# Optimization experiments

Hardware: AMD Instinct MI355X
Metric: run time of the kernel (lower is better)

Reference implementation:

```python
import jax, jax.numpy as jnp
import numpy as np

HEADS = 4
HEAD_DIM = 32
IN_DIM = 128
N_TRIG = 48
N_SPAN = 128


def build_edges(T, S):
    # nodes are (trig r, span c) flattened row-major: n = r*S + c
    N = T * S
    nodes = jnp.arange(N, dtype=jnp.int32)
    r = nodes // S
    c = nodes % S
    # same-row neighbors (includes self loop once): [N, S]
    row_nb = r[:, None] * S + jnp.arange(S, dtype=jnp.int32)[None, :]
    # same-column neighbors excluding own row: [N, T-1]
    t_idx = jnp.arange(T - 1, dtype=jnp.int32)[None, :]
    t = t_idx + (t_idx >= r[:, None]).astype(jnp.int32)
    col_nb = t * S + c[:, None]
    deg = S + T - 1
    src = jnp.concatenate([row_nb, col_nb], axis=1).reshape(-1)  # [N*deg]
    dst = jnp.repeat(nodes, deg)
    return src, dst, N


def gat_conv(x, src, dst, N, W, att_src, att_dst, bias):
    # PyG GATConv (eval mode, dropout off), concat=True.
    # W: [in, H*Hd]; att_src/att_dst: [H, Hd]; bias: [H*Hd]
    h = (x @ W).reshape(N, HEADS, HEAD_DIM)          # [N,H,Hd]
    a_src = jnp.sum(h * att_src[None], axis=-1)      # [N,H]
    a_dst = jnp.sum(h * att_dst[None], axis=-1)      # [N,H]
    e = jax.nn.leaky_relu(a_src[src] + a_dst[dst], negative_slope=0.2)  # [E,H]
    # scatter-softmax over incoming edges per destination node
    m = jax.ops.segment_max(e, dst, num_segments=N)  # [N,H]
    ex = jnp.exp(e - m[dst])
    denom = jax.ops.segment_sum(ex, dst, num_segments=N)
    alpha = ex / denom[dst]                          # [E,H]
    msg = alpha[:, :, None] * h[src]                 # [E,H,Hd]
    out = jax.ops.segment_sum(msg, dst, num_segments=N)  # [N,H,Hd]
    return out.reshape(N, HEADS * HEAD_DIM) + bias[None]


def setup_inputs() -> dict:
    key = jax.random.key(0)
    ks = jax.random.split(key, 9)
    D = IN_DIM
    HD = HEADS * HEAD_DIM
    inp = {
        "pair_embeddings": jax.random.normal(ks[0], (1, N_TRIG, N_SPAN, D), dtype=jnp.float32),
        "W1": jax.random.normal(ks[1], (D, HD), dtype=jnp.float32) * (2.0 / (D + HD)) ** 0.5,
        "att_src1": jax.random.normal(ks[2], (HEADS, HEAD_DIM), dtype=jnp.float32) * 0.1,
        "att_dst1": jax.random.normal(ks[3], (HEADS, HEAD_DIM), dtype=jnp.float32) * 0.1,
        "b1": jnp.zeros((HD,), dtype=jnp.float32),
        "W2": jax.random.normal(ks[4], (HD, HD), dtype=jnp.float32) * (2.0 / (HD + HD)) ** 0.5,
        "att_src2": jax.random.normal(ks[5], (HEADS, HEAD_DIM), dtype=jnp.float32) * 0.1,
        "att_dst2": jax.random.normal(ks[6], (HEADS, HEAD_DIM), dtype=jnp.float32) * 0.1,
        "b2": jnp.zeros((HD,), dtype=jnp.float32),
        "num_trigs_kept": N_TRIG,
        "num_arg_spans_kept": N_SPAN,
    }
    return inp


def reference(pair_embeddings, W1, att_src1, att_dst1, b1, W2, att_src2, att_dst2, b2, num_trigs_kept, num_arg_spans_kept):
    T, S = int(num_trigs_kept), int(num_arg_spans_kept)
    src, dst, N = build_edges(T, S)
    # batch_size == 1: slice and flatten node features
    x = pair_embeddings[0, :T, :S].reshape(N, -1)
    x = jax.nn.elu(gat_conv(x, src, dst, N, W1, att_src1, att_dst1, b1))
    x = jax.nn.elu(gat_conv(x, src, dst, N, W2, att_src2, att_dst2, b2))
    return x
```

## Files before the change

kernel.cpp:

```cpp
#include <hip/hip_runtime.h>

#define T_TRIG 48
#define S_SPAN 128
#define NN (T_TRIG * S_SPAN)
#define D 128

__global__ __launch_bounds__(256) void gemm_att_kernel(
    const float* __restrict__ X, const float* __restrict__ W,
    const float* __restrict__ att_s, const float* __restrict__ att_d,
    float* __restrict__ H, float* __restrict__ asrc, float* __restrict__ adst)
{
    const int tid = threadIdx.x;
    const int tx = tid & 15;
    const int ty = tid >> 4;
    const int i0 = blockIdx.x * 32 + ty * 2;
    const int j0 = tx * 8;

    float acc[2][8];
    #pragma unroll
    for (int a = 0; a < 2; ++a)
        #pragma unroll
        for (int b = 0; b < 8; ++b) acc[a][b] = 0.f;

    const float* x0 = X + (size_t)i0 * D;
    #pragma unroll 4
    for (int k = 0; k < D; k += 4) {
        float4 xa4 = *(const float4*)(x0 + k);
        float4 xb4 = *(const float4*)(x0 + D + k);
        float xa[4] = {xa4.x, xa4.y, xa4.z, xa4.w};
        float xb[4] = {xb4.x, xb4.y, xb4.z, xb4.w};
        #pragma unroll
        for (int kk = 0; kk < 4; ++kk) {
            const float* wr = W + (k + kk) * D + j0;
            float4 w0 = *(const float4*)(wr);
            float4 w1 = *(const float4*)(wr + 4);
            float wv[8] = {w0.x, w0.y, w0.z, w0.w, w1.x, w1.y, w1.z, w1.w};
            #pragma unroll
            for (int jj = 0; jj < 8; ++jj) {
                acc[0][jj] = fmaf(xa[kk], wv[jj], acc[0][jj]);
                acc[1][jj] = fmaf(xb[kk], wv[jj], acc[1][jj]);
            }
        }
    }

    #pragma unroll
    for (int ii = 0; ii < 2; ++ii) {
        float4 o0 = {acc[ii][0], acc[ii][1], acc[ii][2], acc[ii][3]};
        float4 o1 = {acc[ii][4], acc[ii][5], acc[ii][6], acc[ii][7]};
        *(float4*)&H[(size_t)(i0 + ii) * D + j0]     = o0;
        *(float4*)&H[(size_t)(i0 + ii) * D + j0 + 4] = o1;
    }

    const int head = tx >> 2;
    const int dbase = head * 32 + (tx & 3) * 8;
    float asv[8], adv[8];
    #pragma unroll
    for (int jj = 0; jj < 8; ++jj) {
        asv[jj] = att_s[dbase + jj];
        adv[jj] = att_d[dbase + jj];
    }
    #pragma unroll
    for (int ii = 0; ii < 2; ++ii) {
        float ps = 0.f, pd = 0.f;
        #pragma unroll
        for (int jj = 0; jj < 8; ++jj) {
            ps = fmaf(acc[ii][jj], asv[jj], ps);
            pd = fmaf(acc[ii][jj], adv[jj], pd);
        }
        ps += __shfl_xor(ps, 1); ps += __shfl_xor(ps, 2);
        pd += __shfl_xor(pd, 1); pd += __shfl_xor(pd, 2);
        if ((tx & 3) == 0) {
            asrc[(i0 + ii) * 4 + head] = ps;
            adst[(i0 + ii) * 4 + head] = pd;
        }
    }
}

__global__ __launch_bounds__(256) void row_agg_kernel(
    const float* __restrict__ H, const float* __restrict__ asrc,
    const float* __restrict__ adst, float* __restrict__ num_row,
    float* __restrict__ den_row)
{
    __shared__ float sh_h[S_SPAN][32];
    __shared__ float sh_as[S_SPAN];
    const int tid = threadIdx.x;
    const int r = blockIdx.x >> 2;
    const int h = blockIdx.x & 3;
    const int base = r * S_SPAN;

    #pragma unroll
    for (int it = 0; it < 4; ++it) {
        int chunk = tid + it * 256;
        int cp = chunk >> 3, fc = chunk & 7;
        *(float4*)&sh_h[cp][fc * 4] =
            *(const float4*)&H[(size_t)(base + cp) * D + h * 32 + fc * 4];
    }
    if (tid < S_SPAN) sh_as[tid] = asrc[(base + tid) * 4 + h];
    __syncthreads();

    const int fg = tid & 3;
    const int cth = tid >> 2;
    const float ad0 = adst[(base + cth) * 4 + h];
    const float ad1 = adst[(base + cth + 64) * 4 + h];
    float4 n00 = {0,0,0,0}, n01 = {0,0,0,0}, n10 = {0,0,0,0}, n11 = {0,0,0,0};
    float den0 = 0.f, den1 = 0.f;

    #pragma unroll 2
    for (int cp = 0; cp < S_SPAN; ++cp) {
        float a = sh_as[cp];
        float4 h0 = *(float4*)&sh_h[cp][fg * 8];
        float4 h1 = *(float4*)&sh_h[cp][fg * 8 + 4];
        float e0 = a + ad0; e0 = fmaxf(e0, 0.2f * e0);
        float e1 = a + ad1; e1 = fmaxf(e1, 0.2f * e1);
        float w0 = __expf(e0);
        float w1 = __expf(e1);
        den0 += w0; den1 += w1;
        n00.x = fmaf(w0, h0.x, n00.x); n00.y = fmaf(w0, h0.y, n00.y);
        n00.z = fmaf(w0, h0.z, n00.z); n00.w = fmaf(w0, h0.w, n00.w);
        n01.x = fmaf(w0, h1.x, n01.x); n01.y = fmaf(w0, h1.y, n01.y);
        n01.z = fmaf(w0, h1.z, n01.z); n01.w = fmaf(w0, h1.w, n01.w);
        n10.x = fmaf(w1, h0.x, n10.x); n10.y = fmaf(w1, h0.y, n10.y);
        n10.z = fmaf(w1, h0.z, n10.z); n10.w = fmaf(w1, h0.w, n10.w);
        n11.x = fmaf(w1, h1.x, n11.x); n11.y = fmaf(w1, h1.y, n11.y);
        n11.z = fmaf(w1, h1.z, n11.z); n11.w = fmaf(w1, h1.w, n11.w);
    }

    const int n0 = base + cth, n1 = n0 + 64;
    *(float4*)&num_row[(size_t)n0 * D + h * 32 + fg * 8]     = n00;
    *(float4*)&num_row[(size_t)n0 * D + h * 32 + fg * 8 + 4] = n01;
    *(float4*)&num_row[(size_t)n1 * D + h * 32 + fg * 8]     = n10;
    *(float4*)&num_row[(size_t)n1 * D + h * 32 + fg * 8 + 4] = n11;
    if (fg == 0) {
        den_row[n0 * 4 + h] = den0;
        den_row[n1 * 4 + h] = den1;
    }
}

__global__ __launch_bounds__(256) void col_agg_kernel(
    const float* __restrict__ H, const float* __restrict__ asrc,
    const float* __restrict__ adst, const float* __restrict__ num_row,
    const float* __restrict__ den_row, const float* __restrict__ bias,
    float* __restrict__ out)
{
    __shared__ float sh_h[T_TRIG][D];
    __shared__ float sh_as[4][T_TRIG];
    const int c = blockIdx.x;
    const int tid = threadIdx.x;

    #pragma unroll
    for (int it = 0; it < 6; ++it) {
        int chunk = tid + it * 256;
        int t = chunk >> 5, fc = chunk & 31;
        *(float4*)&sh_h[t][fc * 4] =
            *(const float4*)&H[(size_t)(t * S_SPAN + c) * D + fc * 4];
    }
    if (tid < 4 * T_TRIG) {
        int hh = tid / T_TRIG, t = tid - hh * T_TRIG;
        sh_as[hh][t] = asrc[(t * S_SPAN + c) * 4 + hh];
    }
    __syncthreads();

    const int f4g = tid & 31;
    const int tg = tid >> 5;
    const int head = f4g >> 3;

    float4 num[6];
    float den[6], ad[6];
    #pragma unroll
    for (int dd = 0; dd < 6; ++dd) {
        num[dd] = {0,0,0,0};
        den[dd] = 0.f;
        ad[dd] = adst[((tg * 6 + dd) * S_SPAN + c) * 4 + head];
    }

    for (int tp = 0; tp < T_TRIG; ++tp) {
        float a = sh_as[head][tp];
        float4 hv = *(float4*)&sh_h[tp][f4g * 4];
        #pragma unroll
        for (int dd = 0; dd < 6; ++dd) {
            float e = a + ad[dd];
            e = fmaxf(e, 0.2f * e);
            float w = __expf(e);
            w = (tp == tg * 6 + dd) ? 0.f : w;
            den[dd] += w;
            num[dd].x = fmaf(w, hv.x, num[dd].x);
            num[dd].y = fmaf(w, hv.y, num[dd].y);
            num[dd].z = fmaf(w, hv.z, num[dd].z);
            num[dd].w = fmaf(w, hv.w, num[dd].w);
        }
    }

    const float4 b4 = *(const float4*)&bias[f4g * 4];
    #pragma unroll
    for (int dd = 0; dd < 6; ++dd) {
        int n = (tg * 6 + dd) * S_SPAN + c;
        float4 nr = *(const float4*)&num_row[(size_t)n * D + f4g * 4];
        float dr = den_row[n * 4 + head];
        float inv = 1.f / (dr + den[dd]);
        float4 o;
        o.x = (nr.x + num[dd].x) * inv + b4.x;
        o.y = (nr.y + num[dd].y) * inv + b4.y;
        o.z = (nr.z + num[dd].z) * inv + b4.z;
        o.w = (nr.w + num[dd].w) * inv + b4.w;
        o.x = o.x > 0.f ? o.x : (__expf(o.x) - 1.f);
        o.y = o.y > 0.f ? o.y : (__expf(o.y) - 1.f);
        o.z = o.z > 0.f ? o.z : (__expf(o.z) - 1.f);
        o.w = o.w > 0.f ? o.w : (__expf(o.w) - 1.f);
        *(float4*)&out[(size_t)n * D + f4g * 4] = o;
    }
}

extern "C" void kernel_launch(void* const* d_in, const int* in_sizes, int n_in,
                              void* d_out, int out_size, void* d_ws, size_t ws_size,
                              hipStream_t stream)
{
    const float* pe  = (const float*)d_in[0];
    const float* W1  = (const float*)d_in[1];
    const float* as1 = (const float*)d_in[2];
    const float* ad1 = (const float*)d_in[3];
    const float* b1  = (const float*)d_in[4];
    const float* W2  = (const float*)d_in[5];
    const float* as2 = (const float*)d_in[6];
    const float* ad2 = (const float*)d_in[7];
    const float* b2  = (const float*)d_in[8];
    float* out = (float*)d_out;

    float* ws = (float*)d_ws;
    float* H     = ws;
    float* X2    = H + (size_t)NN * D;
    float* numr  = X2 + (size_t)NN * D;
    float* asrcb = numr + (size_t)NN * D;
    float* adstb = asrcb + (size_t)NN * 4;
    float* denb  = adstb + (size_t)NN * 4;

    gemm_att_kernel<<<dim3(NN / 32), dim3(256), 0, stream>>>(pe, W1, as1, ad1, H, asrcb, adstb);
    row_agg_kernel<<<dim3(T_TRIG * 4), dim3(256), 0, stream>>>(H, asrcb, adstb, numr, denb);
    col_agg_kernel<<<dim3(S_SPAN), dim3(256), 0, stream>>>(H, asrcb, adstb, numr, denb, b1, X2);
    gemm_att_kernel<<<dim3(NN / 32), dim3(256), 0, stream>>>(X2, W2, as2, ad2, H, asrcb, adstb);
    row_agg_kernel<<<dim3(T_TRIG * 4), dim3(256), 0, stream>>>(H, asrcb, adstb, numr, denb);
    col_agg_kernel<<<dim3(S_SPAN), dim3(256), 0, stream>>>(H, asrcb, adstb, numr, denb, b2, out);
}
```

Measured before the change: 93.97 us.

## Replace FP32 SIMT GEMM with split-bf16 MFMA GEMM and prepacked weights

Replaces the scalar FMA projection GEMM with a matrix-core kernel that uses bf16 MFMA 16x16x32. Each fp32 operand is split into high and low bf16 parts, and three MFMAs per tile recover near-fp32 accuracy. A small pre-pass kernel packs W1 and W2 into an MFMA-friendly layout in the workspace on every call. The attention dot products are then computed from the MFMA accumulators with cross-lane shuffles. The costs are an extra launch, strided scalar stores of H, and slightly lower precision than true fp32.

```diff
diff --git a/kernel.cpp b/kernel.cpp
--- a/kernel.cpp
+++ b/kernel.cpp
@@ -5,73 +5,123 @@
 #define NN (T_TRIG * S_SPAN)
 #define D 128
 
-__global__ __launch_bounds__(256) void gemm_att_kernel(
-    const float* __restrict__ X, const float* __restrict__ W,
+typedef __attribute__((ext_vector_type(8))) short sh8;
+typedef __attribute__((ext_vector_type(4))) float f32x4;
+
+__device__ inline unsigned short f2bf(float v) {
+    unsigned u = __float_as_uint(v);
+    unsigned r = u + 0x7FFFu + ((u >> 16) & 1u);
+    return (unsigned short)(r >> 16);
+}
+__device__ inline float bf2f(unsigned short b) {
+    return __uint_as_float(((unsigned)b) << 16);
+}
+
+__global__ __launch_bounds__(64) void pack_w_kernel(
+    const float* __restrict__ W1, const float* __restrict__ W2,
+    unsigned short* __restrict__ w1h, unsigned short* __restrict__ w1l,
+    unsigned short* __restrict__ w2h, unsigned short* __restrict__ w2l)
+{
+    const int b = blockIdx.x;
+    const int l = threadIdx.x;
+    const float* W = (b < 8) ? W1 : W2;
+    unsigned short* wh = (b < 8) ? w1h : w2h;
+    unsigned short* wl = (b < 8) ? w1l : w2l;
+    const int nt = b & 7;
+    const int n = nt * 16 + (l & 15);
+    const int kgb = (l >> 4) * 8;
+
+    #pragma unroll
+    for (int kc = 0; kc < 4; ++kc) {
+        unsigned short hb[8], lb[8];
+        #pragma unroll
+        for (int i = 0; i < 8; ++i) {
+            int k = kc * 32 + kgb + i;
+            float v = W[k * D + n];
+            unsigned short h = f2bf(v);
+            hb[i] = h;
+            lb[i] = f2bf(v - bf2f(h));
+        }
+        size_t base = ((size_t)(nt * 4 + kc) * 64 + l) * 8;
+        #pragma unroll
+        for (int i = 0; i < 8; ++i) { wh[base + i] = hb[i]; wl[base + i] = lb[i]; }
+    }
+}
+
+__global__ __launch_bounds__(64) void gemm_mfma_kernel(
+    const float* __restrict__ X,
+    const unsigned short* __restrict__ Wh, const unsigned short* __restrict__ Wl,
     const float* __restrict__ att_s, const float* __restrict__ att_d,
     float* __restrict__ H, float* __restrict__ asrc, float* __restrict__ adst)
 {
-    const int tid = threadIdx.x;
-    const int tx = tid & 15;
-    const int ty = tid >> 4;
-    const int i0 = blockIdx.x * 32 + ty * 2;
-    const int j0 = tx * 8;
-
-    float acc[2][8];
-    #pragma unroll
-    for (int a = 0; a < 2; ++a)
-        #pragma unroll
-        for (int b = 0; b < 8; ++b) acc[a][b] = 0.f;
-
-    const float* x0 = X + (size_t)i0 * D;
-    #pragma unroll 4
-    for (int k = 0; k < D; k += 4) {
-        float4 xa4 = *(const float4*)(x0 + k);
-        float4 xb4 = *(const float4*)(x0 + D + k);
-        float xa[4] = {xa4.x, xa4.y, xa4.z, xa4.w};
-        float xb[4] = {xb4.x, xb4.y, xb4.z, xb4.w};
-        #pragma unroll
-        for (int kk = 0; kk < 4; ++kk) {
-            const float* wr = W + (k + kk) * D + j0;
-            float4 w0 = *(const float4*)(wr);
-            float4 w1 = *(const float4*)(wr + 4);
-            float wv[8] = {w0.x, w0.y, w0.z, w0.w, w1.x, w1.y, w1.z, w1.w};
-            #pragma unroll
-            for (int jj = 0; jj < 8; ++jj) {
-                acc[0][jj] = fmaf(xa[kk], wv[jj], acc[0][jj]);
-                acc[1][jj] = fmaf(xb[kk], wv[jj], acc[1][jj]);
-            }
-        }
-    }
-
-    #pragma unroll
-    for (int ii = 0; ii < 2; ++ii) {
-        float4 o0 = {acc[ii][0], acc[ii][1], acc[ii][2], acc[ii][3]};
-        float4 o1 = {acc[ii][4], acc[ii][5], acc[ii][6], acc[ii][7]};
-        *(float4*)&H[(size_t)(i0 + ii) * D + j0]     = o0;
-        *(float4*)&H[(size_t)(i0 + ii) * D + j0 + 4] = o1;
-    }
-
-    const int head = tx >> 2;
-    const int dbase = head * 32 + (tx & 3) * 8;
-    float asv[8], adv[8];
-    #pragma unroll
-    for (int jj = 0; jj < 8; ++jj) {
-        asv[jj] = att_s[dbase + jj];
-        adv[jj] = att_d[dbase + jj];
-    }
-    #pragma unroll
-    for (int ii = 0; ii < 2; ++ii) {
-        float ps = 0.f, pd = 0.f;
-        #pragma unroll
-        for (int jj = 0; jj < 8; ++jj) {
-            ps = fmaf(acc[ii][jj], asv[jj], ps);
-            pd = fmaf(acc[ii][jj], adv[jj], pd);
-        }
-        ps += __shfl_xor(ps, 1); ps += __shfl_xor(ps, 2);
-        pd += __shfl_xor(pd, 1); pd += __shfl_xor(pd, 2);
-        if ((tx & 3) == 0) {
-            asrc[(i0 + ii) * 4 + head] = ps;
-            adst[(i0 + ii) * 4 + head] = pd;
+    const int l = threadIdx.x;
+    const int mt = blockIdx.x >> 1;
+    const int nh = blockIdx.x & 1;
+    const int c = l & 15;
+    const int kg = l >> 4;
+    const int row0 = mt * 16;
+
+    const sh8* Wh8 = (const sh8*)Wh;
+    const sh8* Wl8 = (const sh8*)Wl;
+
+    f32x4 acc[4] = {f32x4{0,0,0,0}, f32x4{0,0,0,0}, f32x4{0,0,0,0}, f32x4{0,0,0,0}};
+
+    #pragma unroll
+    for (int kc = 0; kc < 4; ++kc) {
+        const float* xp = X + (size_t)(row0 + c) * D + kc * 32 + kg * 8;
+        float4 x0 = *(const float4*)xp;
+        float4 x1 = *(const float4*)(xp + 4);
+        float xs[8] = {x0.x, x0.y, x0.z, x0.w, x1.x, x1.y, x1.z, x1.w};
+        sh8 ah, al;
+        #pragma unroll
+        for (int i = 0; i < 8; ++i) {
+            unsigned short h = f2bf(xs[i]);
+            ah[i] = (short)h;
+            al[i] = (short)f2bf(xs[i] - bf2f(h));
+        }
+        #pragma unroll
+        for (int ntl = 0; ntl < 4; ++ntl) {
+            int ntg = nh * 4 + ntl;
+            sh8 bh = Wh8[(ntg * 4 + kc) * 64 + l];
+            sh8 bl = Wl8[(ntg * 4 + kc) * 64 + l];
+            acc[ntl] = __builtin_amdgcn_mfma_f32_16x16x32_bf16(ah, bh, acc[ntl], 0, 0, 0);
+            acc[ntl] = __builtin_amdgcn_mfma_f32_16x16x32_bf16(al, bh, acc[ntl], 0, 0, 0);
+            acc[ntl] = __builtin_amdgcn_mfma_f32_16x16x32_bf16(ah, bl, acc[ntl], 0, 0, 0);
+        }
+    }
+
+    #pragma unroll
+    for (int ntl = 0; ntl < 4; ++ntl) {
+        #pragma unroll
+        for (int i = 0; i < 4; ++i) {
+            H[(size_t)(row0 + kg * 4 + i) * D + nh * 64 + ntl * 16 + c] = acc[ntl][i];
+        }
+    }
+
+    float asv[4], adv[4];
+    #pragma unroll
+    for (int ntl = 0; ntl < 4; ++ntl) {
+        int d = (nh * 2 + (ntl >> 1)) * 32 + (ntl & 1) * 16 + c;
+        asv[ntl] = att_s[d];
+        adv[ntl] = att_d[d];
+    }
+    #pragma unroll
+    for (int i = 0; i < 4; ++i) {
+        float ps0 = acc[0][i] * asv[0] + acc[1][i] * asv[1];
+        float ps1 = acc[2][i] * asv[2] + acc[3][i] * asv[3];
+        float pd0 = acc[0][i] * adv[0] + acc[1][i] * adv[1];
+        float pd1 = acc[2][i] * adv[2] + acc[3][i] * adv[3];
+        #pragma unroll
+        for (int o = 1; o < 16; o <<= 1) {
+            ps0 += __shfl_xor(ps0, o); ps1 += __shfl_xor(ps1, o);
+            pd0 += __shfl_xor(pd0, o); pd1 += __shfl_xor(pd1, o);
+        }
+        if (c == 0) {
+            int rr = row0 + kg * 4 + i;
+            asrc[rr * 4 + nh * 2 + 0] = ps0;
+            asrc[rr * 4 + nh * 2 + 1] = ps1;
+            adst[rr * 4 + nh * 2 + 0] = pd0;
+            adst[rr * 4 + nh * 2 + 1] = pd1;
         }
     }
 }
@@ -225,18 +275,24 @@
     const float* b2  = (const float*)d_in[8];
     float* out = (float*)d_out;
 
-    float* ws = (float*)d_ws;
-    float* H     = ws;
+    char* ws = (char*)d_ws;
+    float* H     = (float*)ws;
     float* X2    = H + (size_t)NN * D;
     float* numr  = X2 + (size_t)NN * D;
     float* asrcb = numr + (size_t)NN * D;
     float* adstb = asrcb + (size_t)NN * 4;
     float* denb  = adstb + (size_t)NN * 4;
-
-    gemm_att_kernel<<<dim3(NN / 32), dim3(256), 0, stream>>>(pe, W1, as1, ad1, H, asrcb, adstb);
+    unsigned short* w1h = (unsigned short*)(denb + (size_t)NN * 4);
+    unsigned short* w1l = w1h + 128 * 128;
+    unsigned short* w2h = w1l + 128 * 128;
+    unsigned short* w2l = w2h + 128 * 128;
+
+    pack_w_kernel<<<dim3(16), dim3(64), 0, stream>>>(W1, W2, w1h, w1l, w2h, w2l);
+
+    gemm_mfma_kernel<<<dim3(768), dim3(64), 0, stream>>>(pe, w1h, w1l, as1, ad1, H, asrcb, adstb);
     row_agg_kernel<<<dim3(T_TRIG * 4), dim3(256), 0, stream>>>(H, asrcb, adstb, numr, denb);
     col_agg_kernel<<<dim3(S_SPAN), dim3(256), 0, stream>>>(H, asrcb, adstb, numr, denb, b1, X2);
-    gemm_att_kernel<<<dim3(NN / 32), dim3(256), 0, stream>>>(X2, W2, as2, ad2, H, asrcb, adstb);
+    gemm_mfma_kernel<<<dim3(768), dim3(64), 0, stream>>>(X2, w2h, w2l, as2, ad2, H, asrcb, adstb);
     row_agg_kernel<<<dim3(T_TRIG * 4), dim3(256), 0, stream>>>(H, asrcb, adstb, numr, denb);
     col_agg_kernel<<<dim3(S_SPAN), dim3(256), 0, stream>>>(H, asrcb, adstb, numr, denb, b2, out);
 }
```

New measurement: 78.42 us. 1.2x faster.
